# Kernel optimization log

Hardware: AMD Instinct MI355X
Metric: run time of the kernel (lower is better)

## Reference

```python
import jax, jax.numpy as jnp
import numpy as np
import math

DIM = 512
MIN_THRES = -5.0
MAX_THRES = 7.0


def setup_inputs() -> dict:
    key = jax.random.key(0)
    k1, k2, k3, k4, k5 = jax.random.split(key, 5)
    s_len, batch, dim = 256, 256, DIM
    x = jax.random.normal(k1, (s_len, batch, dim), dtype=jnp.float32)
    # Linear(dim, dim, bias=False) weights, torch convention y = x @ W.T
    Wq = jax.random.normal(k2, (dim, dim), dtype=jnp.float32) * 0.02
    Wk = jax.random.normal(k3, (dim, dim), dtype=jnp.float32) * 0.02
    Wv = jax.random.normal(k4, (dim, dim), dtype=jnp.float32) * 0.02
    root_query = jax.random.normal(k5, (dim,), dtype=jnp.float32)
    return {"x": x, "Wq": Wq, "Wk": Wk, "Wv": Wv, "root_query": root_query}


def _matrix_tree(score):
    # score: [b, s, s]. Batched matrix-tree theorem marginals (lengths=None -> full length).
    b, s, _ = score.shape
    eye = jnp.eye(s, dtype=score.dtype)
    A = jnp.exp(score)                                  # exp(input)
    rd = jnp.exp(jnp.diagonal(score, axis1=1, axis2=2))  # exp(diag) root scores [b, s]
    L_off = A * (1.0 - eye)                              # mask diagonal
    colsum = L_off.sum(axis=1)                           # lap.sum(0): column sums [b, s]
    lap = -L_off + eye * colsum[:, None, :]              # -A_off + diag(colsum)
    lap = lap.at[:, 0, :].set(rd)                        # lap[0] = exp(diag(input))
    inv = jnp.linalg.inv(lap)                            # [b, s, s]
    inv_diag = jnp.diagonal(inv, axis1=1, axis2=2)       # [b, s]
    term1 = A * inv_diag[:, None, :]                     # factor[i,j] = inv_diag[j]
    term2 = A * jnp.swapaxes(inv, 1, 2)
    term1 = term1.at[:, :, 0].set(0.0)
    term2 = term2.at[:, 0, :].set(0.0)
    roots = rd * inv[:, :, 0]                            # diag(input).exp() * inv.T[0]
    return term1 - term2 + roots[:, :, None] * eye       # [b, s, s]


def reference(x, Wq, Wk, Wv, root_query):
    s_len, batch, dim = x.shape
    scale = math.sqrt(1.0 / dim)
    xt = jnp.swapaxes(x, 0, 1)                           # [b, s, d]
    q = jnp.einsum('bsd,ed->bse', xt, Wq)
    k = jnp.einsum('bsd,ed->bse', xt, Wk)
    v = jnp.einsum('bsd,ed->bse', xt, Wv)
    _score = jnp.einsum('bsd,btd->bst', q, k)            # [b, s, s]
    root = jnp.einsum('bsd,d->bs', k, root_query)        # [b, s]
    eye = jnp.eye(s_len, dtype=x.dtype)
    # Faithful to source: score[b] = _score[b]*eye + diag(root[b]) (off-diagonal zeroed)
    score = _score * eye + root[:, :, None] * eye
    score = jnp.clip(score * scale, MIN_THRES, MAX_THRES)
    edge_score = jnp.swapaxes(_matrix_tree(score), 1, 2)  # [b, s, s]
    return jnp.einsum('bst,btd->bsd', edge_score, v)
```

## Files before the change

kernel.cpp:

```cpp
#include <hip/hip_runtime.h>

typedef __bf16 v8bf __attribute__((ext_vector_type(8)));
typedef float f32x4 __attribute__((ext_vector_type(4)));
typedef unsigned short u16x8 __attribute__((ext_vector_type(8)));

#define SLEN 256
#define BATCH 256
#define DIM 512
#define SCALE 0.044194173824159216f

#define TS 64
#define LDX 520
#define LDB 72
#define KC 64

#define MFMA(a, b, c) __builtin_amdgcn_mfma_f32_16x16x32_bf16((a), (b), (c), 0, 0, 0)

__device__ __forceinline__ unsigned short f2bf(float f) {
  union { float f; unsigned int u; } v; v.f = f;
  unsigned int r = v.u + 0x7FFFu + ((v.u >> 16) & 1u);
  return (unsigned short)(r >> 16);
}
__device__ __forceinline__ float bf2f(unsigned short u) {
  union { unsigned int u; float f; } v; v.u = ((unsigned int)u) << 16;
  return v.f;
}
__device__ __forceinline__ v8bf ld8(const unsigned short* p) {
  u16x8 t = *reinterpret_cast<const u16x8*>(p);
  return __builtin_bit_cast(v8bf, t);
}
__device__ __forceinline__ void gload16(const unsigned short* g, unsigned short* l) {
  __builtin_amdgcn_global_load_lds(
      (const __attribute__((address_space(1))) unsigned int*)g,
      (__attribute__((address_space(3))) unsigned int*)l, 16, 0, 0);
}

__global__ __launch_bounds__(256) void zf(float4* __restrict__ p, int n4) {
  const int i = blockIdx.x * 256 + threadIdx.x;
  if (i < n4) {
    const float4 z = {0.f, 0.f, 0.f, 0.f};
    p[i] = z;
  }
}

__global__ __launch_bounds__(256) void prep_mt(const float* __restrict__ Wq,
                                               const float* __restrict__ Wk,
                                               unsigned short* __restrict__ Mt) {
  __shared__ float As[32][33];
  __shared__ float Bs[32][33];
  const int e0 = (blockIdx.x & 15) * 32;
  const int d0 = (blockIdx.x >> 4) * 32;
  const int tid = threadIdx.x;
  const int tm = (tid & 15) * 2;
  const int tn = (tid >> 4) * 2;
  const int lf = tid >> 3;
  const int lc = (tid & 7) * 4;
  float a00 = 0.f, a01 = 0.f, a10 = 0.f, a11 = 0.f;
  for (int f0 = 0; f0 < DIM; f0 += 32) {
    __syncthreads();
    const float4 a = *reinterpret_cast<const float4*>(Wk + (size_t)(f0 + lf) * DIM + e0 + lc);
    const float4 b = *reinterpret_cast<const float4*>(Wq + (size_t)(f0 + lf) * DIM + d0 + lc);
    As[lf][lc] = a.x; As[lf][lc + 1] = a.y; As[lf][lc + 2] = a.z; As[lf][lc + 3] = a.w;
    Bs[lf][lc] = b.x; Bs[lf][lc + 1] = b.y; Bs[lf][lc + 2] = b.z; Bs[lf][lc + 3] = b.w;
    __syncthreads();
#pragma unroll
    for (int k = 0; k < 32; ++k) {
      const float x0 = As[k][tm], x1 = As[k][tm + 1];
      const float y0 = Bs[k][tn], y1 = Bs[k][tn + 1];
      a00 += x0 * y0; a01 += x0 * y1; a10 += x1 * y0; a11 += x1 * y1;
    }
  }
  Mt[(size_t)(e0 + tm) * DIM + d0 + tn] = f2bf(a00);
  Mt[(size_t)(e0 + tm) * DIM + d0 + tn + 1] = f2bf(a01);
  Mt[(size_t)(e0 + tm + 1) * DIM + d0 + tn] = f2bf(a10);
  Mt[(size_t)(e0 + tm + 1) * DIM + d0 + tn + 1] = f2bf(a11);
}

__global__ __launch_bounds__(256) void conv_wv(const float* __restrict__ Wv,
                                               unsigned short* __restrict__ Wvb) {
  const int idx = (blockIdx.x * 256 + threadIdx.x) * 4;
  const float4 v = *reinterpret_cast<const float4*>(Wv + idx);
  uint2 p;
  p.x = (unsigned int)f2bf(v.x) | ((unsigned int)f2bf(v.y) << 16);
  p.y = (unsigned int)f2bf(v.z) | ((unsigned int)f2bf(v.w) << 16);
  *reinterpret_cast<uint2*>(Wvb + idx) = p;
}

__global__ __launch_bounds__(256) void wkr_k3(const float* __restrict__ Wk,
                                              const float* __restrict__ rq,
                                              float* __restrict__ wkr) {
  const int f0 = blockIdx.x * 32;
  const int d = threadIdx.x;
  float s1 = 0.f, s2 = 0.f;
#pragma unroll
  for (int f = f0; f < f0 + 32; ++f) {
    const float r = rq[f];
    s1 += Wk[(size_t)f * DIM + d] * r;
    s2 += Wk[(size_t)f * DIM + d + 256] * r;
  }
  atomicAdd(&wkr[d], s1);
  atomicAdd(&wkr[d + 256], s2);
}

__global__ __launch_bounds__(256) void wkr_k2(const float* __restrict__ Wk,
                                              const float* __restrict__ rq,
                                              float* __restrict__ wkr) {
  __shared__ float rqs[DIM];
  const int tid = threadIdx.x;
  rqs[tid] = rq[tid];
  rqs[tid + 256] = rq[tid + 256];
  __syncthreads();
  const int d = blockIdx.x * 256 + tid;
  float s = 0.f;
#pragma unroll 8
  for (int f = 0; f < DIM; ++f) s += Wk[(size_t)f * DIM + d] * rqs[f];
  wkr[d] = s;
}

__global__ __launch_bounds__(256) void x2b(const float* __restrict__ X,
                                           unsigned short* __restrict__ Xb,
                                           float* __restrict__ xsump) {
  const int b = blockIdx.x & 255;
  const int sc = blockIdx.x >> 8;
  const int s0 = sc * 64;
  const int tid = threadIdx.x;
  const int half = tid >> 7;
  const int d0 = (tid & 127) * 4;
  float4 xs = {0.f, 0.f, 0.f, 0.f};
  for (int ib = 0; ib < 32; ib += 8) {
    float4 v[8];
#pragma unroll
    for (int u = 0; u < 8; ++u) {
      const int s = s0 + 2 * (ib + u) + half;
      v[u] = *reinterpret_cast<const float4*>(X + ((size_t)s * BATCH + b) * DIM + d0);
    }
#pragma unroll
    for (int u = 0; u < 8; ++u) {
      const int s = s0 + 2 * (ib + u) + half;
      uint2 p;
      p.x = (unsigned int)f2bf(v[u].x) | ((unsigned int)f2bf(v[u].y) << 16);
      p.y = (unsigned int)f2bf(v[u].z) | ((unsigned int)f2bf(v[u].w) << 16);
      *reinterpret_cast<uint2*>(Xb + ((size_t)b * SLEN + s) * DIM + d0) = p;
      xs.x += v[u].x; xs.y += v[u].y; xs.z += v[u].z; xs.w += v[u].w;
    }
  }
  *reinterpret_cast<float4*>(xsump + ((size_t)b * 8 + sc * 2 + half) * DIM + d0) = xs;
}


#define GEMM_PIPE_LOOP(EXTRA_NONE)                                              \
  f32x4 acc[8][4] = {};                                                         \
  STG(0); STG(1); STG(2);                                                       \
  for (int t = 0; t < 16; ++t) {                                                \
    if (t <= 13) { asm volatile("s_waitcnt vmcnt(8)" ::: "memory"); }           \
    else if (t == 14) { asm volatile("s_waitcnt vmcnt(4)" ::: "memory"); }      \
    else { asm volatile("s_waitcnt vmcnt(0)" ::: "memory"); }                   \
    __builtin_amdgcn_s_barrier();                                               \
    __builtin_amdgcn_sched_barrier(0);                                          \
    if (t + 3 < 16) { STG(t + 3); }                                             \
    __builtin_amdgcn_sched_barrier(0);                                          \
    const unsigned short* la = lds + (t & 3) * 16384;                           \
    const unsigned short* lb2 = la + 8192;                                      \
    v8bf a[8], bbf[4];                                                          \
    _Pragma("unroll")                                                           \
    for (int m = 0; m < 8; ++m)                                                 \
      a[m] = ld8(la + (wr * 128 + m * 16 + c) * 32 + grd);                      \
    _Pragma("unroll")                                                           \
    for (int n = 0; n < 4; ++n)                                                 \
      bbf[n] = ld8(lb2 + (wc * 64 + n * 16 + c) * 32 + grd);                    \
    __builtin_amdgcn_s_setprio(1);                                              \
    _Pragma("unroll")                                                           \
    for (int m = 0; m < 8; ++m)                                                 \
      _Pragma("unroll")                                                         \
      for (int n = 0; n < 4; ++n) acc[m][n] = MFMA(a[m], bbf[n], acc[m][n]);    \
    __builtin_amdgcn_s_setprio(0);                                              \
  }

#define STG(tt) {                                                               \
    const int kc_ = (tt) * 32;                                                  \
    unsigned short* lb_ = lw + ((tt) & 3) * 16384;                              \
    gload16(sAp + kc_, lb_);                                                    \
    gload16(sAp + kc_ + 128 * DIM, lb_ + 4096);                                 \
    gload16(sBp + kc_, lb_ + 8192);                                             \
    gload16(sBp + kc_ + 128 * DIM, lb_ + 12288); }

__global__ __launch_bounds__(512, 2) void gemm1_dp(const unsigned short* __restrict__ Xb,
                                                   const unsigned short* __restrict__ Mt,
                                                   const float* __restrict__ wkr,
                                                   float* __restrict__ rdpart) {
  __shared__ unsigned short lds[65536];
  const int tid = threadIdx.x;
  const int lane = tid & 63, w = tid >> 6;
  const int wr = w >> 2, wc = w & 3;
  const int c = lane & 15, g = lane >> 4;
  const int grd = ((g ^ ((c >> 1) & 3))) * 8;

  const int work = (blockIdx.x & 7) * 64 + (blockIdx.x >> 3);
  const int rt = work >> 1, ct = work & 1;
  const int j0 = rt * 256, e0 = ct * 256;

  const int rA = tid >> 2;
  const int gl = (tid & 3) ^ ((rA >> 1) & 3);
  const unsigned short* sAp = Xb + (size_t)(j0 + rA) * DIM + gl * 8;
  const unsigned short* sBp = Mt + (size_t)(e0 + rA) * DIM + gl * 8;
  unsigned short* lw = lds + (w << 9);

  GEMM_PIPE_LOOP(0)

  float wkrl[4];
#pragma unroll
  for (int n = 0; n < 4; ++n) wkrl[n] = wkr[e0 + wc * 64 + n * 16 + c];
#pragma unroll
  for (int m = 0; m < 8; ++m) {
#pragma unroll
    for (int i = 0; i < 4; ++i) {
      const int r = wr * 128 + m * 16 + 4 * g + i;
      const unsigned short* xrow = Xb + (size_t)(j0 + r) * DIM + e0 + wc * 64 + c;
      float val = 0.f;
#pragma unroll
      for (int n = 0; n < 4; ++n)
        val += (acc[m][n][i] + wkrl[n]) * bf2f(xrow[n * 16]);
      val += __shfl_xor(val, 1); val += __shfl_xor(val, 2);
      val += __shfl_xor(val, 4); val += __shfl_xor(val, 8);
      if (c == 0) atomicAdd(&rdpart[(size_t)j0 + r], val);
    }
  }
}

__global__ __launch_bounds__(512, 2) void gemm2_dp(const unsigned short* __restrict__ Xb,
                                                   const unsigned short* __restrict__ Wvb,
                                                   const float* __restrict__ rd,
                                                   const float* __restrict__ Rsum,
                                                   const float* __restrict__ c2,
                                                   float* __restrict__ out) {
  __shared__ unsigned short lds[65536];
  const int tid = threadIdx.x;
  const int lane = tid & 63, w = tid >> 6;
  const int wr = w >> 2, wc = w & 3;
  const int c = lane & 15, g = lane >> 4;
  const int grd = ((g ^ ((c >> 1) & 3))) * 8;

  const int work = (blockIdx.x & 7) * 64 + (blockIdx.x >> 3);
  const int rt = work >> 1, ct = work & 1;
  const int j0 = rt * 256, e0 = ct * 256;
  const int b = rt;

  const int rA = tid >> 2;
  const int gl = (tid & 3) ^ ((rA >> 1) & 3);
  const unsigned short* sAp = Xb + (size_t)(j0 + rA) * DIM + gl * 8;
  const unsigned short* sBp = Wvb + (size_t)(e0 + rA) * DIM + gl * 8;
  unsigned short* lw = lds + (w << 9);

  GEMM_PIPE_LOOP(0)

  const float invR = 1.0f / Rsum[b];
  const float gam = invR * 0.00390625f;
  float vssl[4], vwsl[4];
#pragma unroll
  for (int n = 0; n < 4; ++n) {
    const int cl = e0 + wc * 64 + n * 16 + c;
    vssl[n] = c2[(size_t)b * DIM + cl];
    vwsl[n] = c2[(size_t)(BATCH + b) * DIM + cl];
  }
#pragma unroll
  for (int m = 0; m < 8; ++m) {
#pragma unroll
    for (int i = 0; i < 4; ++i) {
      const int r = wr * 128 + m * 16 + 4 * g + i;
      const float tt = rd[(size_t)b * SLEN + r] * invR;
      const float al = tt - 0.00390625f;
      const float be = (1.0f - tt) * 0.00390625f;
      float* orow = out + (size_t)(j0 + r) * DIM + e0 + wc * 64 + c;
#pragma unroll
      for (int n = 0; n < 4; ++n)
        orow[n * 16] = al * acc[m][n][i] + be * vssl[n] + gam * vwsl[n];
    }
  }
}

__global__ __launch_bounds__(256) void fixup1(const float* __restrict__ rdpart,
                                              const float* __restrict__ xsump,
                                              float* __restrict__ rd, float* __restrict__ Rsum,
                                              float* __restrict__ u2) {
  __shared__ float wsum[4];
  const int b = blockIdx.x, tid = threadIdx.x;
  float v = rdpart[(size_t)b * SLEN + tid] * SCALE;
  v = fminf(fmaxf(v, -5.0f), 7.0f);
  const float r = expf(v);
  rd[(size_t)b * SLEN + tid] = r;
  float t = r;
  t += __shfl_xor(t, 1);  t += __shfl_xor(t, 2);  t += __shfl_xor(t, 4);
  t += __shfl_xor(t, 8);  t += __shfl_xor(t, 16); t += __shfl_xor(t, 32);
  if ((tid & 63) == 0) wsum[tid >> 6] = t;
  __syncthreads();
  if (tid == 0) Rsum[b] = wsum[0] + wsum[1] + wsum[2] + wsum[3];

  const int d0 = 2 * tid;
  float2 xs = {0.f, 0.f};
#pragma unroll
  for (int ch = 0; ch < 8; ++ch) {
    const float2 p = *reinterpret_cast<const float2*>(xsump + ((size_t)b * 8 + ch) * DIM + d0);
    xs.x += p.x; xs.y += p.y;
  }
  *reinterpret_cast<float2*>(u2 + (size_t)b * DIM + d0) = xs;
}

__global__ __launch_bounds__(256) void xwk(const unsigned short* __restrict__ Xb,
                                           const float* __restrict__ rd,
                                           float* __restrict__ u2) {
  __shared__ float rds[64];
  const int b = blockIdx.x & 255;
  const int sc = blockIdx.x >> 8;
  const int s0 = sc * 64;
  const int tid = threadIdx.x;
  if (tid < 64) rds[tid] = rd[(size_t)b * SLEN + s0 + tid];
  __syncthreads();
  const int d0 = 2 * tid;
  float a0 = 0.f, a1 = 0.f;
  for (int rb = 0; rb < 64; rb += 8) {
    unsigned int p[8];
#pragma unroll
    for (int u = 0; u < 8; ++u)
      p[u] = *reinterpret_cast<const unsigned int*>(
          Xb + ((size_t)b * SLEN + s0 + rb + u) * DIM + d0);
#pragma unroll
    for (int u = 0; u < 8; ++u) {
      const float rr = rds[rb + u];
      a0 += rr * bf2f((unsigned short)(p[u] & 0xffffu));
      a1 += rr * bf2f((unsigned short)(p[u] >> 16));
    }
  }
  atomicAdd(&u2[(size_t)(BATCH + b) * DIM + d0], a0);
  atomicAdd(&u2[(size_t)(BATCH + b) * DIM + d0 + 1], a1);
}

__global__ __launch_bounds__(256) void vsvw(const float* __restrict__ u2,
                                            const float* __restrict__ Wv,
                                            float* __restrict__ c2) {
  __shared__ float Us[32][33];
  __shared__ float Ws[32][33];
  const int r0 = (blockIdx.x & 15) * 32;
  const int e0 = (blockIdx.x >> 4) * 32;
  const int tid = threadIdx.x;
  const int tm = (tid & 15) * 2;
  const int tn = (tid >> 4) * 2;
  const int lf = tid >> 3;
  const int lc = (tid & 7) * 4;
  float a00 = 0.f, a01 = 0.f, a10 = 0.f, a11 = 0.f;
  for (int k0 = 0; k0 < DIM; k0 += 32) {
    __syncthreads();
    const float4 a = *reinterpret_cast<const float4*>(u2 + (size_t)(r0 + lf) * DIM + k0 + lc);
    const float4 w = *reinterpret_cast<const float4*>(Wv + (size_t)(e0 + lf) * DIM + k0 + lc);
    Us[lf][lc] = a.x; Us[lf][lc + 1] = a.y; Us[lf][lc + 2] = a.z; Us[lf][lc + 3] = a.w;
    Ws[lf][lc] = w.x; Ws[lf][lc + 1] = w.y; Ws[lf][lc + 2] = w.z; Ws[lf][lc + 3] = w.w;
    __syncthreads();
#pragma unroll
    for (int k = 0; k < 32; ++k) {
      const float x0 = Us[tm][k], x1 = Us[tm + 1][k];
      const float y0 = Ws[tn][k], y1 = Ws[tn + 1][k];
      a00 += x0 * y0; a01 += x0 * y1; a10 += x1 * y0; a11 += x1 * y1;
    }
  }
  c2[(size_t)(r0 + tm) * DIM + e0 + tn] = a00;
  c2[(size_t)(r0 + tm) * DIM + e0 + tn + 1] = a01;
  c2[(size_t)(r0 + tm + 1) * DIM + e0 + tn] = a10;
  c2[(size_t)(r0 + tm + 1) * DIM + e0 + tn + 1] = a11;
}

__global__ __launch_bounds__(256, 2) void pass1_fb(
    const float* __restrict__ X, const unsigned short* __restrict__ Mt,
    const float* __restrict__ wkr, float* __restrict__ rd_out,
    float* __restrict__ Rsum, float* __restrict__ xsum, float* __restrict__ xw) {
  __shared__ __align__(16) unsigned short Xs[TS * LDX];
  __shared__ __align__(16) unsigned short Bsh[64 * LDB];
  __shared__ float wkrs[DIM];
  __shared__ float dacc[TS];
  __shared__ float rds[TS];
  const int tid = threadIdx.x;
  const int b = blockIdx.x & 255;
  const int s0 = (blockIdx.x >> 8) * TS;
  const int lane = tid & 63;
  const int wave = tid >> 6;
  const int wr = wave >> 1, wc = wave & 1;
  const int g = lane >> 4, c = lane & 15;
#pragma unroll 4
  for (int r = 0; r < TS; ++r) {
    const float2 v = *reinterpret_cast<const float2*>(
        X + ((size_t)(s0 + r) * BATCH + b) * DIM + tid * 2);
    Xs[r * LDX + tid * 2] = f2bf(v.x);
    Xs[r * LDX + tid * 2 + 1] = f2bf(v.y);
  }
  wkrs[tid] = wkr[tid];
  wkrs[tid + 256] = wkr[tid + 256];
  if (tid < TS) dacc[tid] = 0.f;
  float dp0[4] = {0.f, 0.f, 0.f, 0.f};
  float dp1[4] = {0.f, 0.f, 0.f, 0.f};
  for (int et = 0; et < 8; ++et) {
    const int e0 = et * 64;
    f32x4 acc00 = {0.f,0.f,0.f,0.f}, acc01 = {0.f,0.f,0.f,0.f};
    f32x4 acc10 = {0.f,0.f,0.f,0.f}, acc11 = {0.f,0.f,0.f,0.f};
    for (int kc0 = 0; kc0 < DIM; kc0 += KC) {
      __syncthreads();
      {
        const int e = tid >> 2;
        const int kq = (tid & 3) * 16;
        const uint4* src = reinterpret_cast<const uint4*>(Mt + (size_t)(e0 + e) * DIM + kc0 + kq);
        const uint4 w0 = src[0];
        const uint4 w1 = src[1];
        *reinterpret_cast<uint4*>(&Bsh[e * LDB + kq]) = w0;
        *reinterpret_cast<uint4*>(&Bsh[e * LDB + kq + 8]) = w1;
      }
      __syncthreads();
#pragma unroll
      for (int ks = 0; ks < KC; ks += 32) {
        const int ka = kc0 + ks + 8 * g;
        const int kb = ks + 8 * g;
        const v8bf fa0 = ld8(&Xs[(32 * wr + c) * LDX + ka]);
        const v8bf fa1 = ld8(&Xs[(32 * wr + 16 + c) * LDX + ka]);
        const v8bf fb0 = ld8(&Bsh[(32 * wc + c) * LDB + kb]);
        const v8bf fb1 = ld8(&Bsh[(32 * wc + 16 + c) * LDB + kb]);
        acc00 = MFMA(fa0, fb0, acc00);
        acc01 = MFMA(fa0, fb1, acc01);
        acc10 = MFMA(fa1, fb0, acc10);
        acc11 = MFMA(fa1, fb1, acc11);
      }
    }
#pragma unroll
    for (int i = 0; i < 4; ++i) {
      const int r0 = 32 * wr + 4 * g + i;
      const int ec0 = e0 + 32 * wc + c;
      const float w0 = wkrs[ec0], w1 = wkrs[ec0 + 16];
      dp0[i] += (acc00[i] + w0) * bf2f(Xs[r0 * LDX + ec0]) +
                (acc01[i] + w1) * bf2f(Xs[r0 * LDX + ec0 + 16]);
      dp1[i] += (acc10[i] + w0) * bf2f(Xs[(r0 + 16) * LDX + ec0]) +
                (acc11[i] + w1) * bf2f(Xs[(r0 + 16) * LDX + ec0 + 16]);
    }
  }
#pragma unroll
  for (int i = 0; i < 4; ++i) {
    float v0 = dp0[i], v1 = dp1[i];
    v0 += __shfl_xor(v0, 1); v0 += __shfl_xor(v0, 2);
    v0 += __shfl_xor(v0, 4); v0 += __shfl_xor(v0, 8);
    v1 += __shfl_xor(v1, 1); v1 += __shfl_xor(v1, 2);
    v1 += __shfl_xor(v1, 4); v1 += __shfl_xor(v1, 8);
    if (c == 0) {
      atomicAdd(&dacc[32 * wr + 4 * g + i], v0);
      atomicAdd(&dacc[32 * wr + 16 + 4 * g + i], v1);
    }
  }
  __syncthreads();
  if (tid < TS) {
    float sc = dacc[tid] * SCALE;
    sc = fminf(fmaxf(sc, -5.0f), 7.0f);
    const float r = expf(sc);
    rds[tid] = r;
    rd_out[(size_t)b * SLEN + s0 + tid] = r;
    float t = r;
    t += __shfl_xor(t, 1); t += __shfl_xor(t, 2); t += __shfl_xor(t, 4);
    t += __shfl_xor(t, 8); t += __shfl_xor(t, 16); t += __shfl_xor(t, 32);
    if (tid == 0) atomicAdd(&Rsum[b], t);
  }
  __syncthreads();
#pragma unroll
  for (int dd = 0; dd < 2; ++dd) {
    const int d = tid + dd * 256;
    float s1 = 0.f, s2 = 0.f;
    for (int r = 0; r < TS; ++r) {
      const float xv = bf2f(Xs[r * LDX + d]);
      s1 += xv;
      s2 += rds[r] * xv;
    }
    atomicAdd(&xsum[(size_t)b * DIM + d], s1);
    atomicAdd(&xw[(size_t)b * DIM + d], s2);
  }
}

__global__ __launch_bounds__(256, 2) void pass2_fb(
    const float* __restrict__ X, const unsigned short* __restrict__ Wvb,
    const float* __restrict__ rd, const float* __restrict__ Rsum,
    const float* __restrict__ xsum, const float* __restrict__ xw,
    float* __restrict__ out) {
  __shared__ __align__(16) unsigned short Zs[TS * LDX];
  __shared__ __align__(16) unsigned short Bsh[64 * LDB];
  __shared__ float xss[DIM];
  __shared__ float xws[DIM];
  __shared__ float rds[TS];
  const int tid = threadIdx.x;
  const int b = blockIdx.x & 255;
  const int s0 = (blockIdx.x >> 8) * TS;
  const int lane = tid & 63;
  const int wave = tid >> 6;
  const int wr = wave >> 1, wc = wave & 1;
  const int g = lane >> 4, c = lane & 15;
  xss[tid] = xsum[(size_t)b * DIM + tid];
  xss[tid + 256] = xsum[(size_t)b * DIM + tid + 256];
  xws[tid] = xw[(size_t)b * DIM + tid];
  xws[tid + 256] = xw[(size_t)b * DIM + tid + 256];
  if (tid < TS) rds[tid] = rd[(size_t)b * SLEN + s0 + tid];
  const float Rb = Rsum[b];
  const float invR = 1.0f / Rb;
  const float gam = invR * (1.0f / 256.0f);
  __syncthreads();
#pragma unroll 4
  for (int r = 0; r < TS; ++r) {
    const float rv = rds[r];
    const float al = rv * invR - (1.0f / 256.0f);
    const float be = (1.0f - rv * invR) * (1.0f / 256.0f);
    const float2 v = *reinterpret_cast<const float2*>(
        X + ((size_t)(s0 + r) * BATCH + b) * DIM + tid * 2);
    const int d0 = tid * 2;
    Zs[r * LDX + d0] = f2bf(al * v.x + be * xss[d0] + gam * xws[d0]);
    Zs[r * LDX + d0 + 1] = f2bf(al * v.y + be * xss[d0 + 1] + gam * xws[d0 + 1]);
  }
  const size_t outbase = ((size_t)b * SLEN + s0) * DIM;
  for (int et = 0; et < 8; ++et) {
    const int e0 = et * 64;
    f32x4 acc00 = {0.f,0.f,0.f,0.f}, acc01 = {0.f,0.f,0.f,0.f};
    f32x4 acc10 = {0.f,0.f,0.f,0.f}, acc11 = {0.f,0.f,0.f,0.f};
    for (int kc0 = 0; kc0 < DIM; kc0 += KC) {
      __syncthreads();
      {
        const int e = tid >> 2;
        const int kq = (tid & 3) * 16;
        const uint4* src = reinterpret_cast<const uint4*>(Wvb + (size_t)(e0 + e) * DIM + kc0 + kq);
        const uint4 w0 = src[0];
        const uint4 w1 = src[1];
        *reinterpret_cast<uint4*>(&Bsh[e * LDB + kq]) = w0;
        *reinterpret_cast<uint4*>(&Bsh[e * LDB + kq + 8]) = w1;
      }
      __syncthreads();
#pragma unroll
      for (int ks = 0; ks < KC; ks += 32) {
        const int ka = kc0 + ks + 8 * g;
        const int kb = ks + 8 * g;
        const v8bf fa0 = ld8(&Zs[(32 * wr + c) * LDX + ka]);
        const v8bf fa1 = ld8(&Zs[(32 * wr + 16 + c) * LDX + ka]);
        const v8bf fb0 = ld8(&Bsh[(32 * wc + c) * LDB + kb]);
        const v8bf fb1 = ld8(&Bsh[(32 * wc + 16 + c) * LDB + kb]);
        acc00 = MFMA(fa0, fb0, acc00);
        acc01 = MFMA(fa0, fb1, acc01);
        acc10 = MFMA(fa1, fb0, acc10);
        acc11 = MFMA(fa1, fb1, acc11);
      }
    }
#pragma unroll
    for (int i = 0; i < 4; ++i) {
      const int r0 = 32 * wr + 4 * g + i;
      const int c0 = e0 + 32 * wc + c;
      out[outbase + (size_t)r0 * DIM + c0] = acc00[i];
      out[outbase + (size_t)r0 * DIM + c0 + 16] = acc01[i];
      out[outbase + (size_t)(r0 + 16) * DIM + c0] = acc10[i];
      out[outbase + (size_t)(r0 + 16) * DIM + c0 + 16] = acc11[i];
    }
  }
}

extern "C" void kernel_launch(void* const* d_in, const int* in_sizes, int n_in,
                              void* d_out, int out_size, void* d_ws, size_t ws_size,
                              hipStream_t stream) {
  (void)in_sizes; (void)n_in; (void)out_size;
  const float* X = (const float*)d_in[0];
  const float* Wq = (const float*)d_in[1];
  const float* Wk = (const float*)d_in[2];
  const float* Wv = (const float*)d_in[3];
  const float* rq = (const float*)d_in[4];
  float* out = (float*)d_out;
  char* ws = (char*)d_ws;

  unsigned short* Mt = (unsigned short*)(ws + 0);
  unsigned short* Wvb = (unsigned short*)(ws + 524288);

  const size_t NEED = 74981376;
  if (ws_size >= NEED) {
    float* wkr = (float*)(ws + 1048576);
    float* rdpart = (float*)(ws + 1052672);
    float* u2 = (float*)(ws + 1314816);
    float* c2 = (float*)(ws + 2363392);
    float* rd = (float*)(ws + 3411968);
    float* Rsum = (float*)(ws + 3674112);
    float* xsump = (float*)(ws + 3678208);
    unsigned short* Xb = (unsigned short*)(ws + 7872512);

    zf<<<dim3(321), dim3(256), 0, stream>>>((float4*)(ws + 1048576), 82176);

    prep_mt<<<dim3(256), dim3(256), 0, stream>>>(Wq, Wk, Mt);
    conv_wv<<<dim3(256), dim3(256), 0, stream>>>(Wv, Wvb);
    wkr_k3<<<dim3(16), dim3(256), 0, stream>>>(Wk, rq, wkr);
    x2b<<<dim3(1024), dim3(256), 0, stream>>>(X, Xb, xsump);
    gemm1_dp<<<dim3(512), dim3(512), 0, stream>>>(Xb, Mt, wkr, rdpart);
    fixup1<<<dim3(256), dim3(256), 0, stream>>>(rdpart, xsump, rd, Rsum, u2);
    xwk<<<dim3(1024), dim3(256), 0, stream>>>(Xb, rd, u2);
    vsvw<<<dim3(256), dim3(256), 0, stream>>>(u2, Wv, c2);
    gemm2_dp<<<dim3(512), dim3(512), 0, stream>>>(Xb, Wvb, rd, Rsum, c2, out);
  } else {
    float* rd = (float*)(ws + 1048576);
    float* wkr = (float*)(ws + 1310720);
    float* Rsum = (float*)(ws + 1312768);
    float* xsum = (float*)(ws + 1313792);
    float* xw = (float*)(ws + 1838080);
    zf<<<dim3(257), dim3(256), 0, stream>>>((float4*)(ws + 1310720), 65728);
    prep_mt<<<dim3(256), dim3(256), 0, stream>>>(Wq, Wk, Mt);
    conv_wv<<<dim3(256), dim3(256), 0, stream>>>(Wv, Wvb);
    wkr_k2<<<dim3(2), dim3(256), 0, stream>>>(Wk, rq, wkr);
    pass1_fb<<<dim3(1024), dim3(256), 0, stream>>>(X, Mt, wkr, rd, Rsum, xsum, xw);
    pass2_fb<<<dim3(1024), dim3(256), 0, stream>>>(X, Wvb, rd, Rsum, xsum, xw, out);
  }
}
```

Measured before the change: 223.4 us.

## Fuse prep kernels and fold vs/vw reductions into the value GEMM epilogue

The separate prep kernels (X to bf16, Wq^T·Wk product, Wv conversion, Wk·rq) are merged into one block-partitioned launch, and the zeroing kernel is removed. gemm1 now reduces its partial root scores through LDS and writes them per column tile instead of using atomics. The fixup, xwk and vsvw kernels are dropped: gemm2 recomputes exp(clipped root), the row sum, and the column sums vs/vw directly from its own accumulators via shuffles and LDS. This cuts launches and intermediate global traffic, at the cost of extra reduction work and barriers in the GEMM epilogues.

Measured after the change: 187.0 us. -16.3%, faster.

```diff
diff --git a/kernel.cpp b/kernel.cpp
--- a/kernel.cpp
+++ b/kernel.cpp
@@ -43,114 +43,95 @@
   }
 }
 
-__global__ __launch_bounds__(256) void prep_mt(const float* __restrict__ Wq,
-                                               const float* __restrict__ Wk,
-                                               unsigned short* __restrict__ Mt) {
+__global__ __launch_bounds__(256) void prep_all(const float* __restrict__ X,
+                                                const float* __restrict__ Wq,
+                                                const float* __restrict__ Wk,
+                                                const float* __restrict__ Wv,
+                                                const float* __restrict__ rq,
+                                                unsigned short* __restrict__ Xb,
+                                                unsigned short* __restrict__ Mt,
+                                                unsigned short* __restrict__ Wvb,
+                                                float* __restrict__ wkr) {
   __shared__ float As[32][33];
   __shared__ float Bs[32][33];
-  const int e0 = (blockIdx.x & 15) * 32;
-  const int d0 = (blockIdx.x >> 4) * 32;
-  const int tid = threadIdx.x;
-  const int tm = (tid & 15) * 2;
-  const int tn = (tid >> 4) * 2;
-  const int lf = tid >> 3;
-  const int lc = (tid & 7) * 4;
-  float a00 = 0.f, a01 = 0.f, a10 = 0.f, a11 = 0.f;
-  for (int f0 = 0; f0 < DIM; f0 += 32) {
+  const int blk = blockIdx.x;
+  const int tid = threadIdx.x;
+
+  if (blk < 1024) {
+    const int b = blk & 255;
+    const int sc = blk >> 8;
+    const int s0 = sc * 64;
+    const int half = tid >> 7;
+    const int d0 = (tid & 127) * 4;
+    for (int ib = 0; ib < 32; ib += 8) {
+      float4 v[8];
+#pragma unroll
+      for (int u = 0; u < 8; ++u) {
+        const int s = s0 + 2 * (ib + u) + half;
+        v[u] = *reinterpret_cast<const float4*>(X + ((size_t)s * BATCH + b) * DIM + d0);
+      }
+#pragma unroll
+      for (int u = 0; u < 8; ++u) {
+        const int s = s0 + 2 * (ib + u) + half;
+        uint2 p;
+        p.x = (unsigned int)f2bf(v[u].x) | ((unsigned int)f2bf(v[u].y) << 16);
+        p.y = (unsigned int)f2bf(v[u].z) | ((unsigned int)f2bf(v[u].w) << 16);
+        *reinterpret_cast<uint2*>(Xb + ((size_t)b * SLEN + s) * DIM + d0) = p;
+      }
+    }
+  } else if (blk < 1280) {
+    const int bid = blk - 1024;
+    const int e0 = (bid & 15) * 32;
+    const int d0 = (bid >> 4) * 32;
+    const int tm = (tid & 15) * 2;
+    const int tn = (tid >> 4) * 2;
+    const int lf = tid >> 3;
+    const int lc = (tid & 7) * 4;
+    float a00 = 0.f, a01 = 0.f, a10 = 0.f, a11 = 0.f;
+    for (int f0 = 0; f0 < DIM; f0 += 32) {
+      __syncthreads();
+      const float4 a = *reinterpret_cast<const float4*>(Wk + (size_t)(f0 + lf) * DIM + e0 + lc);
+      const float4 b = *reinterpret_cast<const float4*>(Wq + (size_t)(f0 + lf) * DIM + d0 + lc);
+      As[lf][lc] = a.x; As[lf][lc + 1] = a.y; As[lf][lc + 2] = a.z; As[lf][lc + 3] = a.w;
+      Bs[lf][lc] = b.x; Bs[lf][lc + 1] = b.y; Bs[lf][lc + 2] = b.z; Bs[lf][lc + 3] = b.w;
+      __syncthreads();
+#pragma unroll
+      for (int k = 0; k < 32; ++k) {
+        const float x0 = As[k][tm], x1 = As[k][tm + 1];
+        const float y0 = Bs[k][tn], y1 = Bs[k][tn + 1];
+        a00 += x0 * y0; a01 += x0 * y1; a10 += x1 * y0; a11 += x1 * y1;
+      }
+    }
+    Mt[(size_t)(e0 + tm) * DIM + d0 + tn] = f2bf(a00);
+    Mt[(size_t)(e0 + tm) * DIM + d0 + tn + 1] = f2bf(a01);
+    Mt[(size_t)(e0 + tm + 1) * DIM + d0 + tn] = f2bf(a10);
+    Mt[(size_t)(e0 + tm + 1) * DIM + d0 + tn + 1] = f2bf(a11);
+  } else if (blk < 1536) {
+    const int idx = ((blk - 1280) * 256 + tid) * 4;
+    const float4 v = *reinterpret_cast<const float4*>(Wv + idx);
+    uint2 p;
+    p.x = (unsigned int)f2bf(v.x) | ((unsigned int)f2bf(v.y) << 16);
+    p.y = (unsigned int)f2bf(v.z) | ((unsigned int)f2bf(v.w) << 16);
+    *reinterpret_cast<uint2*>(Wvb + idx) = p;
+  } else {
+    float* rqs = &As[0][0];
+    rqs[tid] = rq[tid];
+    rqs[tid + 256] = rq[tid + 256];
     __syncthreads();
-    const float4 a = *reinterpret_cast<const float4*>(Wk + (size_t)(f0 + lf) * DIM + e0 + lc);
-    const float4 b = *reinterpret_cast<const float4*>(Wq + (size_t)(f0 + lf) * DIM + d0 + lc);
-    As[lf][lc] = a.x; As[lf][lc + 1] = a.y; As[lf][lc + 2] = a.z; As[lf][lc + 3] = a.w;
-    Bs[lf][lc] = b.x; Bs[lf][lc + 1] = b.y; Bs[lf][lc + 2] = b.z; Bs[lf][lc + 3] = b.w;
-    __syncthreads();
-#pragma unroll
-    for (int k = 0; k < 32; ++k) {
-      const float x0 = As[k][tm], x1 = As[k][tm + 1];
-      const float y0 = Bs[k][tn], y1 = Bs[k][tn + 1];
-      a00 += x0 * y0; a01 += x0 * y1; a10 += x1 * y0; a11 += x1 * y1;
-    }
-  }
-  Mt[(size_t)(e0 + tm) * DIM + d0 + tn] = f2bf(a00);
-  Mt[(size_t)(e0 + tm) * DIM + d0 + tn + 1] = f2bf(a01);
-  Mt[(size_t)(e0 + tm + 1) * DIM + d0 + tn] = f2bf(a10);
-  Mt[(size_t)(e0 + tm + 1) * DIM + d0 + tn + 1] = f2bf(a11);
-}
-
-__global__ __launch_bounds__(256) void conv_wv(const float* __restrict__ Wv,
-                                               unsigned short* __restrict__ Wvb) {
-  const int idx = (blockIdx.x * 256 + threadIdx.x) * 4;
-  const float4 v = *reinterpret_cast<const float4*>(Wv + idx);
-  uint2 p;
-  p.x = (unsigned int)f2bf(v.x) | ((unsigned int)f2bf(v.y) << 16);
-  p.y = (unsigned int)f2bf(v.z) | ((unsigned int)f2bf(v.w) << 16);
-  *reinterpret_cast<uint2*>(Wvb + idx) = p;
-}
-
-__global__ __launch_bounds__(256) void wkr_k3(const float* __restrict__ Wk,
-                                              const float* __restrict__ rq,
-                                              float* __restrict__ wkr) {
-  const int f0 = blockIdx.x * 32;
-  const int d = threadIdx.x;
-  float s1 = 0.f, s2 = 0.f;
-#pragma unroll
-  for (int f = f0; f < f0 + 32; ++f) {
-    const float r = rq[f];
-    s1 += Wk[(size_t)f * DIM + d] * r;
-    s2 += Wk[(size_t)f * DIM + d + 256] * r;
-  }
-  atomicAdd(&wkr[d], s1);
-  atomicAdd(&wkr[d + 256], s2);
-}
-
-__global__ __launch_bounds__(256) void wkr_k2(const float* __restrict__ Wk,
-                                              const float* __restrict__ rq,
-                                              float* __restrict__ wkr) {
-  __shared__ float rqs[DIM];
-  const int tid = threadIdx.x;
-  rqs[tid] = rq[tid];
-  rqs[tid + 256] = rq[tid + 256];
-  __syncthreads();
-  const int d = blockIdx.x * 256 + tid;
-  float s = 0.f;
+    const int d = (blk - 1536) * 256 + tid;
+    float s = 0.f;
 #pragma unroll 8
-  for (int f = 0; f < DIM; ++f) s += Wk[(size_t)f * DIM + d] * rqs[f];
-  wkr[d] = s;
-}
-
-__global__ __launch_bounds__(256) void x2b(const float* __restrict__ X,
-                                           unsigned short* __restrict__ Xb,
-                                           float* __restrict__ xsump) {
-  const int b = blockIdx.x & 255;
-  const int sc = blockIdx.x >> 8;
-  const int s0 = sc * 64;
-  const int tid = threadIdx.x;
-  const int half = tid >> 7;
-  const int d0 = (tid & 127) * 4;
-  float4 xs = {0.f, 0.f, 0.f, 0.f};
-  for (int ib = 0; ib < 32; ib += 8) {
-    float4 v[8];
-#pragma unroll
-    for (int u = 0; u < 8; ++u) {
-      const int s = s0 + 2 * (ib + u) + half;
-      v[u] = *reinterpret_cast<const float4*>(X + ((size_t)s * BATCH + b) * DIM + d0);
-    }
-#pragma unroll
-    for (int u = 0; u < 8; ++u) {
-      const int s = s0 + 2 * (ib + u) + half;
-      uint2 p;
-      p.x = (unsigned int)f2bf(v[u].x) | ((unsigned int)f2bf(v[u].y) << 16);
-      p.y = (unsigned int)f2bf(v[u].z) | ((unsigned int)f2bf(v[u].w) << 16);
-      *reinterpret_cast<uint2*>(Xb + ((size_t)b * SLEN + s) * DIM + d0) = p;
-      xs.x += v[u].x; xs.y += v[u].y; xs.z += v[u].z; xs.w += v[u].w;
-    }
-  }
-  *reinterpret_cast<float4*>(xsump + ((size_t)b * 8 + sc * 2 + half) * DIM + d0) = xs;
-}
-
-
-#define GEMM_PIPE_LOOP(EXTRA_NONE)                                              \
+    for (int f = 0; f < DIM; ++f) s += Wk[(size_t)f * DIM + d] * rqs[f];
+    wkr[d] = s;
+  }
+}
+
+
+#define GEMM_PROLOGUE()                                                         \
   f32x4 acc[8][4] = {};                                                         \
-  STG(0); STG(1); STG(2);                                                       \
+  STG(0); STG(1); STG(2);
+
+#define GEMM_MAIN_LOOP()                                                        \
   for (int t = 0; t < 16; ++t) {                                                \
     if (t <= 13) { asm volatile("s_waitcnt vmcnt(8)" ::: "memory"); }           \
     else if (t == 14) { asm volatile("s_waitcnt vmcnt(4)" ::: "memory"); }      \
@@ -205,8 +186,11 @@
   const unsigned short* sBp = Mt + (size_t)(e0 + rA) * DIM + gl * 8;
   unsigned short* lw = lds + (w << 9);
 
-  GEMM_PIPE_LOOP(0)
-
+  GEMM_PROLOGUE()
+  GEMM_MAIN_LOOP()
+
+  __syncthreads();
+  float* red = (float*)lds;
   float wkrl[4];
 #pragma unroll
   for (int n = 0; n < 4; ++n) wkrl[n] = wkr[e0 + wc * 64 + n * 16 + c];
@@ -214,26 +198,31 @@
   for (int m = 0; m < 8; ++m) {
 #pragma unroll
     for (int i = 0; i < 4; ++i) {
-      const int r = wr * 128 + m * 16 + 4 * g + i;
-      const unsigned short* xrow = Xb + (size_t)(j0 + r) * DIM + e0 + wc * 64 + c;
+      const int rl = wr * 128 + m * 16 + 4 * g + i;
+      const unsigned short* xrow = Xb + (size_t)(j0 + rl) * DIM + e0 + wc * 64 + c;
       float val = 0.f;
 #pragma unroll
       for (int n = 0; n < 4; ++n)
         val += (acc[m][n][i] + wkrl[n]) * bf2f(xrow[n * 16]);
       val += __shfl_xor(val, 1); val += __shfl_xor(val, 2);
       val += __shfl_xor(val, 4); val += __shfl_xor(val, 8);
-      if (c == 0) atomicAdd(&rdpart[(size_t)j0 + r], val);
-    }
-  }
-}
-
-__global__ __launch_bounds__(512, 2) void gemm2_dp(const unsigned short* __restrict__ Xb,
-                                                   const unsigned short* __restrict__ Wvb,
-                                                   const float* __restrict__ rd,
-                                                   const float* __restrict__ Rsum,
-                                                   const float* __restrict__ c2,
-                                                   float* __restrict__ out) {
+      if (c == 0) red[wc * 256 + rl] = val;
+    }
+  }
+  __syncthreads();
+  if (tid < 256) {
+    const float s = red[tid] + red[256 + tid] + red[512 + tid] + red[768 + tid];
+    rdpart[(size_t)ct * 65536 + j0 + tid] = s;
+  }
+}
+
+__global__ __launch_bounds__(512, 2) void gemm2_f(const unsigned short* __restrict__ Xb,
+                                                  const unsigned short* __restrict__ Wvb,
+                                                  const float* __restrict__ rdpart,
+                                                  float* __restrict__ out) {
   __shared__ unsigned short lds[65536];
+  __shared__ float rdl[256];
+  __shared__ float wsum[4];
   const int tid = threadIdx.x;
   const int lane = tid & 63, w = tid >> 6;
   const int wr = w >> 2, wc = w & 3;
@@ -244,6 +233,18 @@
   const int rt = work >> 1, ct = work & 1;
   const int j0 = rt * 256, e0 = ct * 256;
   const int b = rt;
+
+  if (tid < 256) {
+    float v = (rdpart[(size_t)b * SLEN + tid] + rdpart[65536 + (size_t)b * SLEN + tid]) * SCALE;
+    v = fminf(fmaxf(v, -5.0f), 7.0f);
+    const float r = expf(v);
+    rdl[tid] = r;
+    float t = r;
+    t += __shfl_xor(t, 1);  t += __shfl_xor(t, 2);  t += __shfl_xor(t, 4);
+    t += __shfl_xor(t, 8);  t += __shfl_xor(t, 16); t += __shfl_xor(t, 32);
+    if ((tid & 63) == 0) wsum[tid >> 6] = t;
+  }
+  __syncthreads();
 
   const int rA = tid >> 2;
   const int gl = (tid & 3) ^ ((rA >> 1) & 3);
@@ -251,120 +252,120 @@
   const unsigned short* sBp = Wvb + (size_t)(e0 + rA) * DIM + gl * 8;
   unsigned short* lw = lds + (w << 9);
 
-  GEMM_PIPE_LOOP(0)
-
-  const float invR = 1.0f / Rsum[b];
+  GEMM_PROLOGUE()
+  GEMM_MAIN_LOOP()
+
+  float vsp[4] = {0.f, 0.f, 0.f, 0.f}, vwp[4] = {0.f, 0.f, 0.f, 0.f};
+#pragma unroll
+  for (int m = 0; m < 8; ++m) {
+#pragma unroll
+    for (int i = 0; i < 4; ++i) {
+      const int rl = wr * 128 + m * 16 + 4 * g + i;
+      const float rr = rdl[rl];
+#pragma unroll
+      for (int n = 0; n < 4; ++n) {
+        vsp[n] += acc[m][n][i];
+        vwp[n] += rr * acc[m][n][i];
+      }
+    }
+  }
+#pragma unroll
+  for (int n = 0; n < 4; ++n) {
+    vsp[n] += __shfl_xor(vsp[n], 16); vsp[n] += __shfl_xor(vsp[n], 32);
+    vwp[n] += __shfl_xor(vwp[n], 16); vwp[n] += __shfl_xor(vwp[n], 32);
+  }
+  __syncthreads();
+  float* red = (float*)lds;
+  if (g == 0) {
+#pragma unroll
+    for (int n = 0; n < 4; ++n) {
+      red[(w * 4 + n) * 16 + c] = vsp[n];
+      red[512 + (w * 4 + n) * 16 + c] = vwp[n];
+    }
+  }
+  __syncthreads();
+  const float Rb = wsum[0] + wsum[1] + wsum[2] + wsum[3];
+  const float invR = 1.0f / Rb;
   const float gam = invR * 0.00390625f;
-  float vssl[4], vwsl[4];
+  const int wo = w ^ 4;
+  float vsf[4], vwf[4];
 #pragma unroll
   for (int n = 0; n < 4; ++n) {
-    const int cl = e0 + wc * 64 + n * 16 + c;
-    vssl[n] = c2[(size_t)b * DIM + cl];
-    vwsl[n] = c2[(size_t)(BATCH + b) * DIM + cl];
+    vsf[n] = red[(w * 4 + n) * 16 + c] + red[(wo * 4 + n) * 16 + c];
+    vwf[n] = red[512 + (w * 4 + n) * 16 + c] + red[512 + (wo * 4 + n) * 16 + c];
   }
 #pragma unroll
   for (int m = 0; m < 8; ++m) {
 #pragma unroll
     for (int i = 0; i < 4; ++i) {
-      const int r = wr * 128 + m * 16 + 4 * g + i;
-      const float tt = rd[(size_t)b * SLEN + r] * invR;
+      const int rl = wr * 128 + m * 16 + 4 * g + i;
+      const float tt = rdl[rl] * invR;
       const float al = tt - 0.00390625f;
       const float be = (1.0f - tt) * 0.00390625f;
-      float* orow = out + (size_t)(j0 + r) * DIM + e0 + wc * 64 + c;
+      float* orow = out + (size_t)(j0 + rl) * DIM + e0 + wc * 64 + c;
 #pragma unroll
       for (int n = 0; n < 4; ++n)
-        orow[n * 16] = al * acc[m][n][i] + be * vssl[n] + gam * vwsl[n];
-    }
-  }
-}
-
-__global__ __launch_bounds__(256) void fixup1(const float* __restrict__ rdpart,
-                                              const float* __restrict__ xsump,
-                                              float* __restrict__ rd, float* __restrict__ Rsum,
-                                              float* __restrict__ u2) {
-  __shared__ float wsum[4];
-  const int b = blockIdx.x, tid = threadIdx.x;
-  float v = rdpart[(size_t)b * SLEN + tid] * SCALE;
-  v = fminf(fmaxf(v, -5.0f), 7.0f);
-  const float r = expf(v);
-  rd[(size_t)b * SLEN + tid] = r;
-  float t = r;
-  t += __shfl_xor(t, 1);  t += __shfl_xor(t, 2);  t += __shfl_xor(t, 4);
-  t += __shfl_xor(t, 8);  t += __shfl_xor(t, 16); t += __shfl_xor(t, 32);
-  if ((tid & 63) == 0) wsum[tid >> 6] = t;
-  __syncthreads();
-  if (tid == 0) Rsum[b] = wsum[0] + wsum[1] + wsum[2] + wsum[3];
-
-  const int d0 = 2 * tid;
-  float2 xs = {0.f, 0.f};
-#pragma unroll
-  for (int ch = 0; ch < 8; ++ch) {
-    const float2 p = *reinterpret_cast<const float2*>(xsump + ((size_t)b * 8 + ch) * DIM + d0);
-    xs.x += p.x; xs.y += p.y;
-  }
-  *reinterpret_cast<float2*>(u2 + (size_t)b * DIM + d0) = xs;
-}
-
-__global__ __launch_bounds__(256) void xwk(const unsigned short* __restrict__ Xb,
-                                           const float* __restrict__ rd,
-                                           float* __restrict__ u2) {
-  __shared__ float rds[64];
-  const int b = blockIdx.x & 255;
-  const int sc = blockIdx.x >> 8;
-  const int s0 = sc * 64;
-  const int tid = threadIdx.x;
-  if (tid < 64) rds[tid] = rd[(size_t)b * SLEN + s0 + tid];
-  __syncthreads();
-  const int d0 = 2 * tid;
-  float a0 = 0.f, a1 = 0.f;
-  for (int rb = 0; rb < 64; rb += 8) {
-    unsigned int p[8];
-#pragma unroll
-    for (int u = 0; u < 8; ++u)
-      p[u] = *reinterpret_cast<const unsigned int*>(
-          Xb + ((size_t)b * SLEN + s0 + rb + u) * DIM + d0);
-#pragma unroll
-    for (int u = 0; u < 8; ++u) {
-      const float rr = rds[rb + u];
-      a0 += rr * bf2f((unsigned short)(p[u] & 0xffffu));
-      a1 += rr * bf2f((unsigned short)(p[u] >> 16));
-    }
-  }
-  atomicAdd(&u2[(size_t)(BATCH + b) * DIM + d0], a0);
-  atomicAdd(&u2[(size_t)(BATCH + b) * DIM + d0 + 1], a1);
-}
-
-__global__ __launch_bounds__(256) void vsvw(const float* __restrict__ u2,
-                                            const float* __restrict__ Wv,
-                                            float* __restrict__ c2) {
-  __shared__ float Us[32][33];
-  __shared__ float Ws[32][33];
-  const int r0 = (blockIdx.x & 15) * 32;
-  const int e0 = (blockIdx.x >> 4) * 32;
+        orow[n * 16] = al * acc[m][n][i] + be * vsf[n] + gam * vwf[n];
+    }
+  }
+}
+
+__global__ __launch_bounds__(256) void prep_mt(const float* __restrict__ Wq,
+                                               const float* __restrict__ Wk,
+                                               unsigned short* __restrict__ Mt) {
+  __shared__ float As[32][33];
+  __shared__ float Bs[32][33];
+  const int e0 = (blockIdx.x & 15) * 32;
+  const int d0 = (blockIdx.x >> 4) * 32;
   const int tid = threadIdx.x;
   const int tm = (tid & 15) * 2;
   const int tn = (tid >> 4) * 2;
   const int lf = tid >> 3;
   const int lc = (tid & 7) * 4;
   float a00 = 0.f, a01 = 0.f, a10 = 0.f, a11 = 0.f;
-  for (int k0 = 0; k0 < DIM; k0 += 32) {
+  for (int f0 = 0; f0 < DIM; f0 += 32) {
     __syncthreads();
-    const float4 a = *reinterpret_cast<const float4*>(u2 + (size_t)(r0 + lf) * DIM + k0 + lc);
-    const float4 w = *reinterpret_cast<const float4*>(Wv + (size_t)(e0 + lf) * DIM + k0 + lc);
-    Us[lf][lc] = a.x; Us[lf][lc + 1] = a.y; Us[lf][lc + 2] = a.z; Us[lf][lc + 3] = a.w;
-    Ws[lf][lc] = w.x; Ws[lf][lc + 1] = w.y; Ws[lf][lc + 2] = w.z; Ws[lf][lc + 3] = w.w;
+    const float4 a = *reinterpret_cast<const float4*>(Wk + (size_t)(f0 + lf) * DIM + e0 + lc);
+    const float4 b = *reinterpret_cast<const float4*>(Wq + (size_t)(f0 + lf) * DIM + d0 + lc);
+    As[lf][lc] = a.x; As[lf][lc + 1] = a.y; As[lf][lc + 2] = a.z; As[lf][lc + 3] = a.w;
+    Bs[lf][lc] = b.x; Bs[lf][lc + 1] = b.y; Bs[lf][lc + 2] = b.z; Bs[lf][lc + 3] = b.w;
     __syncthreads();
 #pragma unroll
     for (int k = 0; k < 32; ++k) {
-      const float x0 = Us[tm][k], x1 = Us[tm + 1][k];
-      const float y0 = Ws[tn][k], y1 = Ws[tn + 1][k];
+      const float x0 = As[k][tm], x1 = As[k][tm + 1];
+      const float y0 = Bs[k][tn], y1 = Bs[k][tn + 1];
       a00 += x0 * y0; a01 += x0 * y1; a10 += x1 * y0; a11 += x1 * y1;
     }
   }
-  c2[(size_t)(r0 + tm) * DIM + e0 + tn] = a00;
-  c2[(size_t)(r0 + tm) * DIM + e0 + tn + 1] = a01;
-  c2[(size_t)(r0 + tm + 1) * DIM + e0 + tn] = a10;
-  c2[(size_t)(r0 + tm + 1) * DIM + e0 + tn + 1] = a11;
+  Mt[(size_t)(e0 + tm) * DIM + d0 + tn] = f2bf(a00);
+  Mt[(size_t)(e0 + tm) * DIM + d0 + tn + 1] = f2bf(a01);
+  Mt[(size_t)(e0 + tm + 1) * DIM + d0 + tn] = f2bf(a10);
+  Mt[(size_t)(e0 + tm + 1) * DIM + d0 + tn + 1] = f2bf(a11);
+}
+
+__global__ __launch_bounds__(256) void conv_wv(const float* __restrict__ Wv,
+                                               unsigned short* __restrict__ Wvb) {
+  const int idx = (blockIdx.x * 256 + threadIdx.x) * 4;
+  const float4 v = *reinterpret_cast<const float4*>(Wv + idx);
+  uint2 p;
+  p.x = (unsigned int)f2bf(v.x) | ((unsigned int)f2bf(v.y) << 16);
+  p.y = (unsigned int)f2bf(v.z) | ((unsigned int)f2bf(v.w) << 16);
+  *reinterpret_cast<uint2*>(Wvb + idx) = p;
+}
+
+__global__ __launch_bounds__(256) void wkr_k2(const float* __restrict__ Wk,
+                                              const float* __restrict__ rq,
+                                              float* __restrict__ wkr) {
+  __shared__ float rqs[DIM];
+  const int tid = threadIdx.x;
+  rqs[tid] = rq[tid];
+  rqs[tid + 256] = rq[tid + 256];
+  __syncthreads();
+  const int d = blockIdx.x * 256 + tid;
+  float s = 0.f;
+#pragma unroll 8
+  for (int f = 0; f < DIM; ++f) s += Wk[(size_t)f * DIM + d] * rqs[f];
+  wkr[d] = s;
 }
 
 __global__ __launch_bounds__(256, 2) void pass1_fb(
@@ -570,28 +571,15 @@
   unsigned short* Mt = (unsigned short*)(ws + 0);
   unsigned short* Wvb = (unsigned short*)(ws + 524288);
 
-  const size_t NEED = 74981376;
+  const size_t NEED = 69206016;
   if (ws_size >= NEED) {
     float* wkr = (float*)(ws + 1048576);
     float* rdpart = (float*)(ws + 1052672);
-    float* u2 = (float*)(ws + 1314816);
-    float* c2 = (float*)(ws + 2363392);
-    float* rd = (float*)(ws + 3411968);
-    float* Rsum = (float*)(ws + 3674112);
-    float* xsump = (float*)(ws + 3678208);
-    unsigned short* Xb = (unsigned short*)(ws + 7872512);
-
-    zf<<<dim3(321), dim3(256), 0, stream>>>((float4*)(ws + 1048576), 82176);
-
-    prep_mt<<<dim3(256), dim3(256), 0, stream>>>(Wq, Wk, Mt);
-    conv_wv<<<dim3(256), dim3(256), 0, stream>>>(Wv, Wvb);
-    wkr_k3<<<dim3(16), dim3(256), 0, stream>>>(Wk, rq, wkr);
-    x2b<<<dim3(1024), dim3(256), 0, stream>>>(X, Xb, xsump);
+    unsigned short* Xb = (unsigned short*)(ws + 2097152);
+
+    prep_all<<<dim3(1538), dim3(256), 0, stream>>>(X, Wq, Wk, Wv, rq, Xb, Mt, Wvb, wkr);
     gemm1_dp<<<dim3(512), dim3(512), 0, stream>>>(Xb, Mt, wkr, rdpart);
-    fixup1<<<dim3(256), dim3(256), 0, stream>>>(rdpart, xsump, rd, Rsum, u2);
-    xwk<<<dim3(1024), dim3(256), 0, stream>>>(Xb, rd, u2);
-    vsvw<<<dim3(256), dim3(256), 0, stream>>>(u2, Wv, c2);
-    gemm2_dp<<<dim3(512), dim3(512), 0, stream>>>(Xb, Wvb, rd, Rsum, c2, out);
+    gemm2_f<<<dim3(512), dim3(512), 0, stream>>>(Xb, Wvb, rdpart, out);
   } else {
     float* rd = (float*)(ws + 1048576);
     float* wkr = (float*)(ws + 1310720);
```
